# Optimization experiments

Measured on AMD Instinct MI355X. Metric: run time of the kernel, lower is better.

The kernel has to match this reference:

```python
import jax, jax.numpy as jnp
import numpy as np

EPS = 1e-6
N_HEADS = 16
N_KV_HEADS = 4
HEAD_DIM = 128
DIM = 2048
SEQ = 2048
BATCH = 2


def _make_freqs_cis(seqlen, head_dim, theta=10000.0):
    inv = 1.0 / (theta ** (jnp.arange(0, head_dim, 2, dtype=jnp.float32) / head_dim))  # [hd/2]
    t = jnp.arange(seqlen, dtype=jnp.float32)
    ang = jnp.outer(t, inv)  # [seq, hd/2]
    return jnp.stack([jnp.cos(ang), jnp.sin(ang)], axis=-1)  # [seq, hd/2, 2]


def setup_inputs() -> dict:
    key = jax.random.key(0)
    k1, k2, k3 = jax.random.split(key, 3)
    std = 0.02
    x = jax.random.normal(k1, (BATCH, SEQ, DIM), dtype=jnp.float32)
    freqs_cis = _make_freqs_cis(SEQ, HEAD_DIM)
    norm_w = jnp.ones((DIM,), dtype=jnp.float32)
    wqkv_w = jax.random.normal(k2, ((N_HEADS + 2 * N_KV_HEADS) * HEAD_DIM, DIM), dtype=jnp.float32) * std
    wo_w = jax.random.normal(k3, (DIM, N_HEADS * HEAD_DIM), dtype=jnp.float32) * std
    return {"x": x, "freqs_cis": freqs_cis, "norm_w": norm_w, "wqkv_w": wqkv_w, "wo_w": wo_w}


def _rope(t, cos, sin):
    # t: [b, s, h, hd] viewed as pairs; cos/sin: [s, hd/2]
    b, s, h, hd = t.shape
    tr = t.reshape(b, s, h, hd // 2, 2)
    xr, xi = tr[..., 0], tr[..., 1]
    c = cos[None, :, None, :]
    sn = sin[None, :, None, :]
    out_r = xr * c - xi * sn
    out_i = xr * sn + xi * c
    return jnp.stack([out_r, out_i], axis=-1).reshape(b, s, h, hd)


def reference(x, freqs_cis, norm_w, wqkv_w, wo_w):
    bs, seqlen, dim = x.shape
    n_rep = N_HEADS // N_KV_HEADS
    # RMSNorm
    xn = x * jax.lax.rsqrt(jnp.mean(x * x, axis=-1, keepdims=True) + EPS) * norm_w
    # fused QKV projection
    qkv = jnp.einsum('bsd,ed->bse', xn, wqkv_w)
    q_sz = N_HEADS * HEAD_DIM
    kv_sz = N_KV_HEADS * HEAD_DIM
    xq = qkv[..., :q_sz].reshape(bs, seqlen, N_HEADS, HEAD_DIM)
    xk = qkv[..., q_sz:q_sz + kv_sz].reshape(bs, seqlen, N_KV_HEADS, HEAD_DIM)
    xv = qkv[..., q_sz + kv_sz:].reshape(bs, seqlen, N_KV_HEADS, HEAD_DIM)
    cos, sin = freqs_cis[..., 0], freqs_cis[..., 1]
    xq = _rope(xq, cos, sin)
    xk = _rope(xk, cos, sin)
    # GQA: group q heads so kv broadcast replaces repeat_kv materialization
    q = xq.transpose(0, 2, 1, 3).reshape(bs, N_KV_HEADS, n_rep, seqlen, HEAD_DIM)
    k = xk.transpose(0, 2, 1, 3)  # [b, g, s, d]
    v = xv.transpose(0, 2, 1, 3)
    scale = 1.0 / jnp.sqrt(jnp.float32(HEAD_DIM))
    scores = jnp.einsum('bgrqd,bgkd->bgrqk', q, k) * scale
    causal = jnp.tril(jnp.ones((seqlen, seqlen), dtype=bool))
    scores = jnp.where(causal, scores, jnp.finfo(scores.dtype).min)
    probs = jax.nn.softmax(scores, axis=-1)
    out = jnp.einsum('bgrqk,bgkd->bgrqd', probs, v)
    out = out.reshape(bs, N_HEADS, seqlen, HEAD_DIM).transpose(0, 2, 1, 3).reshape(bs, seqlen, N_HEADS * HEAD_DIM)
    return jnp.einsum('bse,de->bsd', out, wo_w)
```

## Files before the change

### kernel.cpp

```cpp
#include <hip/hip_runtime.h>
#include <cstdint>
#include <cstddef>

typedef __bf16 bhalf;
typedef __bf16 bhalf8 __attribute__((ext_vector_type(8)));
typedef __bf16 bhalf4 __attribute__((ext_vector_type(4)));
typedef float f32x4 __attribute__((ext_vector_type(4)));
typedef float f32x16 __attribute__((ext_vector_type(16)));

#define RMS_EPS 1e-6f
#define N_HEADS 16
#define N_KV 4
#define HD 128
#define DIM 2048
#define SEQ 2048
#define BATCH 2

static __device__ __forceinline__ f32x4 mfma16(bhalf8 a, bhalf8 b, f32x4 c) {
    return __builtin_amdgcn_mfma_f32_16x16x32_bf16(a, b, c, 0, 0, 0);
}
static __device__ __forceinline__ f32x16 mfma32(bhalf8 a, bhalf8 b, f32x16 c) {
    return __builtin_amdgcn_mfma_f32_32x32x16_bf16(a, b, c, 0, 0, 0);
}

static __device__ __forceinline__ void gload16(const bhalf* g, bhalf* l) {
    __builtin_amdgcn_global_load_lds((const __attribute__((address_space(1))) unsigned int*)g,
                                     (__attribute__((address_space(3))) unsigned int*)l,
                                     16, 0, 0);
}

static __device__ __forceinline__ unsigned cvt_pk_bf16(float a, float b) {
    unsigned r;
    asm volatile("v_cvt_pk_bf16_f32 %0, %1, %2" : "=v"(r) : "v"(a), "v"(b));
    return r;
}
static __device__ __forceinline__ void plane32_swap(unsigned& a, unsigned& b) {
    asm volatile("v_permlane32_swap_b32 %0, %1" : "+v"(a), "+v"(b));
}

__global__ __launch_bounds__(256) void prep_k(const float* __restrict__ x,
                                              const float* __restrict__ w,
                                              bhalf* __restrict__ xn,
                                              const float* __restrict__ wqkv,
                                              const float* __restrict__ wo,
                                              bhalf* __restrict__ wdst) {
    const int blk = blockIdx.x;
    const int tid = threadIdx.x;
    if (blk < BATCH * SEQ) {
        const int row = blk;
        const float4* xr = (const float4*)(x + (size_t)row * DIM);
        float4 v0 = xr[tid * 2], v1 = xr[tid * 2 + 1];
        float ss = v0.x * v0.x + v0.y * v0.y + v0.z * v0.z + v0.w * v0.w
                 + v1.x * v1.x + v1.y * v1.y + v1.z * v1.z + v1.w * v1.w;
        #pragma unroll
        for (int off = 32; off; off >>= 1) ss += __shfl_xor(ss, off, 64);
        __shared__ float red[4];
        if ((tid & 63) == 0) red[tid >> 6] = ss;
        __syncthreads();
        float tot = red[0] + red[1] + red[2] + red[3];
        float scale = rsqrtf(tot * (1.0f / DIM) + RMS_EPS);
        const float4* wr = (const float4*)w;
        float4 w0 = wr[tid * 2], w1 = wr[tid * 2 + 1];
        bhalf8 o;
        o[0] = (bhalf)(v0.x * scale * w0.x); o[1] = (bhalf)(v0.y * scale * w0.y);
        o[2] = (bhalf)(v0.z * scale * w0.z); o[3] = (bhalf)(v0.w * scale * w0.w);
        o[4] = (bhalf)(v1.x * scale * w1.x); o[5] = (bhalf)(v1.y * scale * w1.y);
        o[6] = (bhalf)(v1.z * scale * w1.z); o[7] = (bhalf)(v1.w * scale * w1.w);
        *(bhalf8*)(xn + (size_t)row * DIM + tid * 8) = o;
    } else {
        size_t i = ((size_t)(blk - BATCH * SEQ) * 256 + tid) * 4;
        const size_t NQ = (size_t)3072 * 2048;
        float4 v = (i < NQ) ? ((const float4*)wqkv)[i >> 2]
                            : ((const float4*)wo)[(i - NQ) >> 2];
        bhalf4 o;
        o[0] = (bhalf)v.x; o[1] = (bhalf)v.y; o[2] = (bhalf)v.z; o[3] = (bhalf)v.w;
        *(bhalf4*)(wdst + i) = o;
    }
}

template <typename OutT>
__global__ __launch_bounds__(512) void gemm8p(const bhalf* __restrict__ A,
                                              const bhalf* __restrict__ B,
                                              OutT* __restrict__ C,
                                              int N, int K) {
    extern __shared__ __align__(16) char smem[];
    const int tid = threadIdx.x;
    const int wid = tid >> 6, lane = tid & 63;
    const int quad = lane >> 4, r16 = lane & 15;
    const int wm = wid >> 2, wn = wid & 3;

    const int nx = N >> 8;
    const int cpx = (int)gridDim.x >> 3;
    const int bs = (int)blockIdx.x;
    const int bid = (bs & 7) * cpx + (bs >> 3);
    const int m0 = (bid / nx) << 8, n0 = (bid % nx) << 8;

    const int srow = wid * 8 + (lane >> 3);
    const int scol = ((lane & 7) ^ ((lane >> 3) & 7)) << 3;
    const bhalf* Asrc = A + (size_t)(m0 + srow) * K + scol;
    const bhalf* Bsrc = B + (size_t)(n0 + srow) * K + scol;
    const size_t r64K = (size_t)64 * K;
    const size_t r128K = (size_t)128 * K;

    const int x7 = r16 & 7;
    const int sl0 = (quad ^ (x7 & 3)) << 4;
    const int ksx = (x7 >> 2) << 6;
    const int k0 = ksx, k1 = 64 ^ ksx;
    const int aoff = (wm << 14) + (r16 << 7) + sl0;
    const int boff = ((2 + (wn >> 1)) << 14) + ((((wn & 1) << 6) + r16) << 7) + sl0;

    f32x4 acc[8][4];
    #pragma unroll
    for (int i = 0; i < 8; ++i)
        #pragma unroll
        for (int j = 0; j < 4; ++j) acc[i][j] = (f32x4)0.0f;

    const int NT = K >> 6;
    const int H = K >> 4;
    int h = 8;

    auto STAGE = [&](int hidx) {
        const int T = hidx >> 2, f = hidx & 3;
        const bhalf* s = ((f < 2) ? Asrc : Bsrc) + ((f & 1) ? r128K : 0) + T * 64;
        char* d = smem + ((T & 1) << 16) + (f << 14) + (wid << 10);
        gload16(s, (bhalf*)d);
        gload16(s + r64K, (bhalf*)(d + 8192));
    };

    #pragma unroll
    for (int i = 0; i < 8; ++i) STAGE(i);
    asm volatile("s_waitcnt vmcnt(8)" ::: "memory");
    __builtin_amdgcn_s_barrier();

    bhalf8 af[4][2], bf[4][2];

    for (int t = 0; t < NT; t += 2) {
        #pragma unroll
        for (int hf = 0; hf < 2; ++hf) {
            char* const bp = smem + (hf << 16);
            #pragma unroll
            for (int i = 0; i < 4; ++i) {
                af[i][0] = *(const bhalf8*)(bp + aoff + i * 2048 + k0);
                af[i][1] = *(const bhalf8*)(bp + aoff + i * 2048 + k1);
            }
            #pragma unroll
            for (int j = 0; j < 2; ++j) {
                bf[j][0] = *(const bhalf8*)(bp + boff + j * 2048 + k0);
                bf[j][1] = *(const bhalf8*)(bp + boff + j * 2048 + k1);
            }
            if ((t > 0 || hf == 1) && h < H) STAGE(h++);
            asm volatile("s_waitcnt lgkmcnt(8)" ::: "memory");
            __builtin_amdgcn_s_barrier();
            __builtin_amdgcn_s_setprio(1);
            #pragma unroll
            for (int i = 0; i < 4; ++i)
                #pragma unroll
                for (int j = 0; j < 2; ++j) {
                    acc[i][j] = mfma16(af[i][0], bf[j][0], acc[i][j]);
                    acc[i][j] = mfma16(af[i][1], bf[j][1], acc[i][j]);
                }
            __builtin_amdgcn_s_setprio(0);
            __builtin_amdgcn_s_barrier();

            #pragma unroll
            for (int j = 2; j < 4; ++j) {
                bf[j][0] = *(const bhalf8*)(bp + boff + j * 2048 + k0);
                bf[j][1] = *(const bhalf8*)(bp + boff + j * 2048 + k1);
            }
            if ((t > 0 || hf == 1) && h < H) STAGE(h++);
            __builtin_amdgcn_s_barrier();
            __builtin_amdgcn_s_setprio(1);
            #pragma unroll
            for (int i = 0; i < 4; ++i)
                #pragma unroll
                for (int j = 2; j < 4; ++j) {
                    acc[i][j] = mfma16(af[i][0], bf[j][0], acc[i][j]);
                    acc[i][j] = mfma16(af[i][1], bf[j][1], acc[i][j]);
                }
            __builtin_amdgcn_s_setprio(0);
            __builtin_amdgcn_s_barrier();

            #pragma unroll
            for (int i = 0; i < 4; ++i) {
                af[i][0] = *(const bhalf8*)(bp + aoff + (i + 4) * 2048 + k0);
                af[i][1] = *(const bhalf8*)(bp + aoff + (i + 4) * 2048 + k1);
            }
            if ((t > 0 || hf == 1) && h < H) STAGE(h++);
            __builtin_amdgcn_s_barrier();
            __builtin_amdgcn_s_setprio(1);
            #pragma unroll
            for (int i = 0; i < 4; ++i)
                #pragma unroll
                for (int j = 0; j < 2; ++j) {
                    acc[i + 4][j] = mfma16(af[i][0], bf[j][0], acc[i + 4][j]);
                    acc[i + 4][j] = mfma16(af[i][1], bf[j][1], acc[i + 4][j]);
                }
            __builtin_amdgcn_s_setprio(0);
            __builtin_amdgcn_s_barrier();

            bool st = (h < H);
            if (st) STAGE(h++);
            __builtin_amdgcn_s_barrier();
            __builtin_amdgcn_s_setprio(1);
            #pragma unroll
            for (int i = 0; i < 4; ++i)
                #pragma unroll
                for (int j = 2; j < 4; ++j) {
                    acc[i + 4][j] = mfma16(af[i][0], bf[j][0], acc[i + 4][j]);
                    acc[i + 4][j] = mfma16(af[i][1], bf[j][1], acc[i + 4][j]);
                }
            __builtin_amdgcn_s_setprio(0);
            if (st) asm volatile("s_waitcnt vmcnt(2)" ::: "memory");
            else    asm volatile("s_waitcnt vmcnt(0)" ::: "memory");
            __builtin_amdgcn_s_barrier();
        }
    }

    #pragma unroll
    for (int i = 0; i < 8; ++i) {
        const int rbase = m0 + wm * 128 + i * 16 + quad * 4;
        #pragma unroll
        for (int rr = 0; rr < 4; ++rr) {
            OutT* crow = C + (size_t)(rbase + rr) * N + n0 + wn * 64 + r16;
            #pragma unroll
            for (int j = 0; j < 4; ++j) crow[j * 16] = (OutT)acc[i][j][rr];
        }
    }
}

template <typename OutT>
__global__ __launch_bounds__(256) void gemm128(const bhalf* __restrict__ A,
                                               const bhalf* __restrict__ B,
                                               OutT* __restrict__ C,
                                               int N, int K) {
    const int tid = threadIdx.x;
    const int w = tid >> 6, lane = tid & 63;
    const int quad = lane >> 4, r16 = lane & 15;
    const int wm = w >> 1, wn = w & 1;

    const int nx = N >> 7;
    const int cpx = (int)gridDim.x >> 3;
    const int bs = (int)blockIdx.x;
    const int bid = (bs & 7) * cpx + (bs >> 3);
    const int m0 = (bid / nx) << 7, n0 = (bid % nx) << 7;

    __shared__ __align__(16) char smem[49152];
    char* const sA = smem;
    char* const sB = smem + 24576;

    const int srow = lane >> 2;
    const int scol = ((lane & 3) ^ (srow & 3)) << 3;
    const bhalf* Ast = A + (size_t)(m0 + w * 16 + srow) * K + scol;
    const bhalf* Bst = B + (size_t)(n0 + w * 16 + srow) * K + scol;
    const size_t r64K = (size_t)64 * K;

    const int xorr = (r16 & 3) << 4;
    const int rdA = (wm * 64 + r16) * 64 + ((quad * 16) ^ xorr);
    const int rdB = (wn * 64 + r16) * 64 + ((quad * 16) ^ xorr);

    f32x4 acc[4][4];
    #pragma unroll
    for (int i = 0; i < 4; ++i)
        #pragma unroll
        for (int j = 0; j < 4; ++j) acc[i][j] = (f32x4)0.0f;

    const int NT = K >> 5;

    #define STG128(t, buf) do {                                                        \
        gload16(Ast + (size_t)(t) * 32,        (bhalf*)(sA + (buf) * 8192 + w * 1024));        \
        gload16(Ast + (size_t)(t) * 32 + r64K, (bhalf*)(sA + (buf) * 8192 + 4096 + w * 1024)); \
        gload16(Bst + (size_t)(t) * 32,        (bhalf*)(sB + (buf) * 8192 + w * 1024));        \
        gload16(Bst + (size_t)(t) * 32 + r64K, (bhalf*)(sB + (buf) * 8192 + 4096 + w * 1024)); \
    } while (0)

    STG128(0, 0);
    STG128(1, 1);

    int cur = 0, c2 = 2;
    for (int t = 0; t < NT; ++t) {
        if (t + 1 < NT) asm volatile("s_waitcnt vmcnt(4)" ::: "memory");
        else            asm volatile("s_waitcnt vmcnt(0)" ::: "memory");
        __builtin_amdgcn_s_barrier();

        char* const bufA = sA + cur * 8192;
        char* const bufB = sB + cur * 8192;
        bhalf8 af[4], bf[4];
        #pragma unroll
        for (int i = 0; i < 4; ++i) af[i] = *(const bhalf8*)(bufA + rdA + i * 1024);
        #pragma unroll
        for (int j = 0; j < 4; ++j) bf[j] = *(const bhalf8*)(bufB + rdB + j * 1024);

        if (t + 2 < NT) STG128(t + 2, c2);

        __builtin_amdgcn_s_setprio(1);
        #pragma unroll
        for (int i = 0; i < 4; ++i)
            #pragma unroll
            for (int j = 0; j < 4; ++j)
                acc[i][j] = mfma16(af[i], bf[j], acc[i][j]);
        __builtin_amdgcn_s_setprio(0);

        cur = (cur == 2) ? 0 : cur + 1;
        c2 = (c2 == 2) ? 0 : c2 + 1;
    }
    #undef STG128

    #pragma unroll
    for (int i = 0; i < 4; ++i) {
        const int rbase = m0 + wm * 64 + i * 16 + quad * 4;
        #pragma unroll
        for (int rr = 0; rr < 4; ++rr) {
            OutT* crow = C + (size_t)(rbase + rr) * N + n0 + wn * 64 + r16;
            #pragma unroll
            for (int j = 0; j < 4; ++j) crow[j * 16] = (OutT)acc[i][j][rr];
        }
    }
}

__global__ __launch_bounds__(256) void rope_k(const bhalf* __restrict__ qkv,
                                              const float* __restrict__ freqs,
                                              bhalf* __restrict__ qb,
                                              bhalf* __restrict__ kb,
                                              bhalf* __restrict__ vt) {
    const int blk = blockIdx.x;
    const int tid = threadIdx.x;
    if (blk < BATCH * SEQ) {
        const int b = blk >> 11, s = blk & 2047;
        const bhalf* row = qkv + (size_t)blk * 3072;
        {
            const int h = tid >> 4, d20 = (tid & 15) * 4;
            bhalf8 e = *(const bhalf8*)(row + h * HD + d20 * 2);
            const float* fp = freqs + (size_t)s * 128 + d20 * 2;
            float4 f0 = *(const float4*)fp;
            float4 f1 = *(const float4*)(fp + 4);
            bhalf8 o;
            o[0] = (bhalf)((float)e[0] * f0.x - (float)e[1] * f0.y);
            o[1] = (bhalf)((float)e[0] * f0.y + (float)e[1] * f0.x);
            o[2] = (bhalf)((float)e[2] * f0.z - (float)e[3] * f0.w);
            o[3] = (bhalf)((float)e[2] * f0.w + (float)e[3] * f0.z);
            o[4] = (bhalf)((float)e[4] * f1.x - (float)e[5] * f1.y);
            o[5] = (bhalf)((float)e[4] * f1.y + (float)e[5] * f1.x);
            o[6] = (bhalf)((float)e[6] * f1.z - (float)e[7] * f1.w);
            o[7] = (bhalf)((float)e[6] * f1.w + (float)e[7] * f1.z);
            *(bhalf8*)(qb + ((size_t)(b * N_HEADS + h) * SEQ + s) * HD + d20 * 2) = o;
        }
        if (tid < 64) {
            const int kh = tid >> 4, d20 = (tid & 15) * 4;
            bhalf8 e = *(const bhalf8*)(row + 2048 + kh * HD + d20 * 2);
            const float* fp = freqs + (size_t)s * 128 + d20 * 2;
            float4 f0 = *(const float4*)fp;
            float4 f1 = *(const float4*)(fp + 4);
            bhalf8 o;
            o[0] = (bhalf)((float)e[0] * f0.x - (float)e[1] * f0.y);
            o[1] = (bhalf)((float)e[0] * f0.y + (float)e[1] * f0.x);
            o[2] = (bhalf)((float)e[2] * f0.z - (float)e[3] * f0.w);
            o[3] = (bhalf)((float)e[2] * f0.w + (float)e[3] * f0.z);
            o[4] = (bhalf)((float)e[4] * f1.x - (float)e[5] * f1.y);
            o[5] = (bhalf)((float)e[4] * f1.y + (float)e[5] * f1.x);
            o[6] = (bhalf)((float)e[6] * f1.z - (float)e[7] * f1.w);
            o[7] = (bhalf)((float)e[6] * f1.w + (float)e[7] * f1.z);
            *(bhalf8*)(kb + ((size_t)(b * N_KV + kh) * SEQ + s) * HD + d20 * 2) = o;
        }
    } else {
        const int vb = blk - BATCH * SEQ;
        const int sc = vb & 31;
        const int kvh = (vb >> 5) & 3;
        const int b = vb >> 7;
        const int s0 = sc * 64;
        __shared__ __align__(16) char lds[64 * 256];

        const int rr = tid >> 4;
        const int slot = tid & 15;
        #pragma unroll
        for (int p = 0; p < 4; ++p) {
            const int s = p * 16 + rr;
            bhalf8 v = *(const bhalf8*)(qkv + (size_t)(b * SEQ + s0 + s) * 3072
                                        + 2560 + kvh * HD + slot * 8);
            *(bhalf8*)(lds + s * 256 + ((slot ^ ((s >> 3) & 7)) << 4)) = v;
        }
        __syncthreads();
        const int j = tid & 7;
        const int d0 = tid >> 3;
        #pragma unroll
        for (int p = 0; p < 4; ++p) {
            const int d = p * 32 + d0;
            bhalf8 o;
            #pragma unroll
            for (int e = 0; e < 8; ++e) {
                const int s = j * 8 + e;
                o[e] = *(const bhalf*)(lds + s * 256 + (((d >> 3) ^ j) << 4) + (d & 7) * 2);
            }
            *(bhalf8*)(vt + ((size_t)(b * N_KV + kvh) * HD + d) * SEQ + s0 + j * 8) = o;
        }
    }
}

__global__ __launch_bounds__(256, 2) void attn_k(const bhalf* __restrict__ qb,
                                                 const bhalf* __restrict__ kb,
                                                 const bhalf* __restrict__ vt,
                                                 bhalf* __restrict__ ob) {
    const int tid = threadIdx.x;
    const int wave = tid >> 6, lane = tid & 63;
    const int l31 = lane & 31, h2 = lane >> 5;
    const int qw = wave & 1, kw = wave >> 1;
    const int bid = ((blockIdx.x & 7) << 6) | ((int)blockIdx.x >> 3);
    const int pair = bid & 15;
    const int hh = (bid >> 4) & 15;
    const int b = bid >> 8;
    const int kvh = hh >> 2;

    __shared__ __align__(16) char smem[33792];
    char* const sK = smem;
    char* const sV = smem + 16384;
    float* const mrg = (float*)smem;

    const bhalf* Kbase = kb + (size_t)(b * N_KV + kvh) * SEQ * HD;
    const bhalf* Vbase = vt + (size_t)(b * N_KV + kvh) * HD * SEQ;
    const float SCL2 = 0.08838834764831845f * 1.4426950408889634f;

    const int mbase = (qw * 64 + lane) * 66;
    const int kr = tid >> 4, kce = (tid & 15) * 8;
    const int vr = tid >> 3, vce = (tid & 7) * 8;
    const int kcB = kce * 2, vcB = vce * 2;
    const int Xl = (h2 << 4) ^ ((l31 & 7) << 4);

    for (int phase = 0; phase < 2; ++phase) {
        const int qt = phase ? (31 - pair) : pair;
        const int qrow = qt * 64 + qw * 32 + l31;
        const int qhi = qt * 64 + qw * 32 + 31;

        const bhalf* qbase = qb + (((size_t)(b * N_HEADS + hh) * SEQ) + qrow) * HD;
        bhalf8 qf[8];
        #pragma unroll
        for (int kk = 0; kk < 8; ++kk) {
            bhalf8 q0 = *(const bhalf8*)(qbase + kk * 16 + h2 * 8);
            #pragma unroll
            for (int e = 0; e < 8; ++e) q0[e] = (bhalf)((float)q0[e] * SCL2);
            qf[kk] = q0;
        }

        f32x16 accO[4];
        #pragma unroll
        for (int dt = 0; dt < 4; ++dt) accO[dt] = (f32x16)0.0f;
        float m_i = -1e30f, l_i = 0.0f;

        bhalf8 kreg[4], vreg[4];
        #pragma unroll
        for (int i = 0; i < 4; ++i) {
            kreg[i] = *(const bhalf8*)(Kbase + (size_t)(kr + 16 * i) * HD + kce);
            vreg[i] = *(const bhalf8*)(Vbase + (size_t)(vr + 32 * i) * SEQ + vce);
        }

        for (int kt = 0; kt <= qt; ++kt) {
            __syncthreads();
            #pragma unroll
            for (int i = 0; i < 4; ++i) {
                const int rk = kr + 16 * i;
                *(bhalf8*)(sK + rk * 256 + (kcB ^ ((rk & 7) << 4))) = kreg[i];
                const int rv = vr + 32 * i;
                *(bhalf8*)(sV + rv * 128 + (vcB ^ ((rv & 7) << 4))) = vreg[i];
            }
            __syncthreads();
            if (kt < qt) {
                const int kn = (kt + 1) * 64;
                #pragma unroll
                for (int i = 0; i < 4; ++i) {
                    kreg[i] = *(const bhalf8*)(Kbase + (size_t)(kn + kr + 16 * i) * HD + kce);
                    vreg[i] = *(const bhalf8*)(Vbase + (size_t)(vr + 32 * i) * SEQ + kn + vce);
                }
            }
            if (qhi < kt * 64 + kw * 32) continue;

            f32x16 accS = (f32x16)0.0f;
            const char* kRow = sK + (kw * 32 + l31) * 256;
            __builtin_amdgcn_s_setprio(1);
            #pragma unroll
            for (int kk = 0; kk < 8; ++kk)
                accS = mfma32(*(const bhalf8*)(kRow + ((kk * 32) ^ Xl)), qf[kk], accS);
            __builtin_amdgcn_s_setprio(0);

            if (kt == qt) {
                #pragma unroll
                for (int r = 0; r < 16; ++r) {
                    const int key = kt * 64 + kw * 32 + (r & 3) + 8 * (r >> 2) + 4 * h2;
                    if (key > qrow) accS[r] = -1e30f;
                }
            }

            float mx = -1e30f;
            #pragma unroll
            for (int r = 0; r < 16; ++r) mx = fmaxf(mx, accS[r]);
            mx = fmaxf(mx, __shfl_xor(mx, 32, 64));

            if (!__all(mx <= m_i + 8.0f)) {
                const float mnew = fmaxf(m_i, mx);
                const float alpha = __builtin_amdgcn_exp2f(m_i - mnew);
                m_i = mnew;
                l_i *= alpha;
                #pragma unroll
                for (int dt = 0; dt < 4; ++dt)
                    #pragma unroll
                    for (int r = 0; r < 16; ++r) accO[dt][r] *= alpha;
            }

            float p[16];
            float rs = 0.0f;
            #pragma unroll
            for (int r = 0; r < 16; ++r) {
                p[r] = __builtin_amdgcn_exp2f(accS[r] - m_i);
                rs += p[r];
            }
            rs += __shfl_xor(rs, 32, 64);
            l_i += rs;

            unsigned X0 = cvt_pk_bf16(p[0],  p[1]);
            unsigned X1 = cvt_pk_bf16(p[2],  p[3]);
            unsigned X2 = cvt_pk_bf16(p[4],  p[5]);
            unsigned X3 = cvt_pk_bf16(p[6],  p[7]);
            unsigned X4 = cvt_pk_bf16(p[8],  p[9]);
            unsigned X5 = cvt_pk_bf16(p[10], p[11]);
            unsigned X6 = cvt_pk_bf16(p[12], p[13]);
            unsigned X7 = cvt_pk_bf16(p[14], p[15]);
            plane32_swap(X0, X2);
            plane32_swap(X1, X3);
            plane32_swap(X4, X6);
            plane32_swap(X5, X7);
            union { unsigned u[8]; bhalf8 h[2]; } pk;
            pk.u[0] = X0; pk.u[1] = X1; pk.u[2] = X2; pk.u[3] = X3;
            pk.u[4] = X4; pk.u[5] = X5; pk.u[6] = X6; pk.u[7] = X7;

            __builtin_amdgcn_s_setprio(1);
            #pragma unroll
            for (int kk2 = 0; kk2 < 2; ++kk2) {
                const int cb = (kw << 6) | (kk2 << 5);
                #pragma unroll
                for (int dt = 0; dt < 4; ++dt) {
                    const bhalf8 vfv = *(const bhalf8*)(sV + (dt * 32 + l31) * 128 + (cb ^ Xl));
                    accO[dt] = mfma32(vfv, pk.h[kk2], accO[dt]);
                }
            }
            __builtin_amdgcn_s_setprio(0);
        }

        __syncthreads();
        if (kw == 1) {
            #pragma unroll
            for (int dt = 0; dt < 4; ++dt)
                #pragma unroll
                for (int r = 0; r < 16; ++r) mrg[mbase + dt * 16 + r] = accO[dt][r];
            mrg[mbase + 64] = m_i;
            mrg[mbase + 65] = l_i;
        }
        __syncthreads();
        if (kw == 0) {
            const float m1 = mrg[mbase + 64];
            const float l1 = mrg[mbase + 65];
            const float m = fmaxf(m_i, m1);
            const float b0 = __builtin_amdgcn_exp2f(m_i - m);
            const float b1 = __builtin_amdgcn_exp2f(m1 - m);
            const float inv = 1.0f / (l_i * b0 + l1 * b1);
            bhalf* obase = ob + ((size_t)b * SEQ + qrow) * (size_t)(N_HEADS * HD) + hh * HD;
            #pragma unroll
            for (int dt = 0; dt < 4; ++dt)
                #pragma unroll
                for (int c = 0; c < 4; ++c) {
                    bhalf4 o4;
                    #pragma unroll
                    for (int rr = 0; rr < 4; ++rr) {
                        const float v = accO[dt][c * 4 + rr] * b0 +
                                        mrg[mbase + dt * 16 + c * 4 + rr] * b1;
                        o4[rr] = (bhalf)(v * inv);
                    }
                    *(bhalf4*)(obase + dt * 32 + c * 8 + h2 * 4) = o4;
                }
        }
    }
}

extern "C" void kernel_launch(void* const* d_in, const int* in_sizes, int n_in,
                              void* d_out, int out_size, void* d_ws, size_t ws_size,
                              hipStream_t stream) {
    const float* x      = (const float*)d_in[0];
    const float* freqs  = (const float*)d_in[1];
    const float* norm_w = (const float*)d_in[2];
    const float* wqkv   = (const float*)d_in[3];
    const float* wo     = (const float*)d_in[4];
    float* out = (float*)d_out;

    char* ws = (char*)d_ws;
    bhalf* wqkv_b = (bhalf*)(ws);
    bhalf* wo_b   = (bhalf*)(ws + 12582912);
    bhalf* xn     = (bhalf*)(ws + 20971520);
    bhalf* qkv    = (bhalf*)(ws + 37748736);
    bhalf* qb     = (bhalf*)(ws + 88080384);
    bhalf* kb     = (bhalf*)(ws + 104857600);
    bhalf* vtb    = (bhalf*)(ws + 109051904);
    bhalf* attn   = (bhalf*)(ws + 113246208);

    static bool attr_done = false;
    if (!attr_done) {
        hipFuncSetAttribute((const void*)gemm8p<bhalf>,
                            hipFuncAttributeMaxDynamicSharedMemorySize, 131072);
        attr_done = true;
    }

    prep_k<<<BATCH * SEQ + 10240, 256, 0, stream>>>(x, norm_w, xn, wqkv, wo, wqkv_b);
    gemm8p<bhalf><<<192, 512, 131072, stream>>>(xn, wqkv_b, qkv, 3072, 2048);
    rope_k<<<BATCH * SEQ + 256, 256, 0, stream>>>(qkv, freqs, qb, kb, vtb);
    attn_k<<<512, 256, 0, stream>>>(qb, kb, vtb, attn);
    gemm128<float><<<512, 256, 0, stream>>>(attn, wo_b, out, 2048, 2048);
}
```

Before: 284.8 us.

## Retile QKV GEMM to 256x192 blocks filling 256 CUs

Replaces the 256x256-tile QKV projection GEMM with a 256x192-tile variant, so the 4096x3072 output maps to 256 blocks instead of 192 and matches the CU count better. The software pipeline is reworked to single-k-tile double buffering with 7 staged loads per tile and new LDS offsets. Each warp now covers 48 columns, which means fewer MFMAs per LDS read and some loss of per-block data reuse.

```diff
diff --git a/kernel.cpp b/kernel.cpp
--- a/kernel.cpp
+++ b/kernel.cpp
@@ -78,142 +78,141 @@
     }
 }
 
-template <typename OutT>
-__global__ __launch_bounds__(512) void gemm8p(const bhalf* __restrict__ A,
-                                              const bhalf* __restrict__ B,
-                                              OutT* __restrict__ C,
-                                              int N, int K) {
+__global__ __launch_bounds__(512) void gemmq(const bhalf* __restrict__ A,
+                                             const bhalf* __restrict__ B,
+                                             bhalf* __restrict__ C,
+                                             int N, int K) {
     extern __shared__ __align__(16) char smem[];
     const int tid = threadIdx.x;
     const int wid = tid >> 6, lane = tid & 63;
     const int quad = lane >> 4, r16 = lane & 15;
     const int wm = wid >> 2, wn = wid & 3;
 
-    const int nx = N >> 8;
+    const int nx = N / 192;
     const int cpx = (int)gridDim.x >> 3;
     const int bs = (int)blockIdx.x;
     const int bid = (bs & 7) * cpx + (bs >> 3);
-    const int m0 = (bid / nx) << 8, n0 = (bid % nx) << 8;
+    const int m0 = (bid / nx) << 8, n0 = (bid % nx) * 192;
 
     const int srow = wid * 8 + (lane >> 3);
     const int scol = ((lane & 7) ^ ((lane >> 3) & 7)) << 3;
     const bhalf* Asrc = A + (size_t)(m0 + srow) * K + scol;
     const bhalf* Bsrc = B + (size_t)(n0 + srow) * K + scol;
-    const size_t r64K = (size_t)64 * K;
-    const size_t r128K = (size_t)128 * K;
 
     const int x7 = r16 & 7;
     const int sl0 = (quad ^ (x7 & 3)) << 4;
     const int ksx = (x7 >> 2) << 6;
     const int k0 = ksx, k1 = 64 ^ ksx;
-    const int aoff = (wm << 14) + (r16 << 7) + sl0;
-    const int boff = ((2 + (wn >> 1)) << 14) + ((((wn & 1) << 6) + r16) << 7) + sl0;
-
-    f32x4 acc[8][4];
+    int aofs[8], bofs[3];
+    #pragma unroll
+    for (int i = 0; i < 8; ++i) {
+        const int g = wm * 128 + i * 16 + r16;
+        aofs[i] = ((g >> 6) << 13) + ((g & 63) << 7) + sl0;
+    }
+    #pragma unroll
+    for (int j = 0; j < 3; ++j) {
+        const int g = wn * 48 + j * 16 + r16;
+        bofs[j] = 32768 + ((g >> 6) << 13) + ((g & 63) << 7) + sl0;
+    }
+
+    auto STG = [&](int T, const bhalf* base, int rowb, int lreg) {
+        gload16(base + (size_t)rowb * K + (size_t)T * 64,
+                (bhalf*)(smem + (T & 1) * 57344 + lreg + wid * 1024));
+    };
+
+    f32x4 acc[8][3];
     #pragma unroll
     for (int i = 0; i < 8; ++i)
         #pragma unroll
-        for (int j = 0; j < 4; ++j) acc[i][j] = (f32x4)0.0f;
+        for (int j = 0; j < 3; ++j) acc[i][j] = (f32x4)0.0f;
 
     const int NT = K >> 6;
-    const int H = K >> 4;
-    int h = 8;
-
-    auto STAGE = [&](int hidx) {
-        const int T = hidx >> 2, f = hidx & 3;
-        const bhalf* s = ((f < 2) ? Asrc : Bsrc) + ((f & 1) ? r128K : 0) + T * 64;
-        char* d = smem + ((T & 1) << 16) + (f << 14) + (wid << 10);
-        gload16(s, (bhalf*)d);
-        gload16(s + r64K, (bhalf*)(d + 8192));
-    };
 
     #pragma unroll
-    for (int i = 0; i < 8; ++i) STAGE(i);
-    asm volatile("s_waitcnt vmcnt(8)" ::: "memory");
+    for (int T = 0; T < 2; ++T) {
+        STG(T, Bsrc, 0, 32768); STG(T, Bsrc, 64, 40960); STG(T, Bsrc, 128, 49152);
+        STG(T, Asrc, 0, 0);     STG(T, Asrc, 128, 16384);
+        STG(T, Asrc, 64, 8192); STG(T, Asrc, 192, 24576);
+    }
+    asm volatile("s_waitcnt vmcnt(7)" ::: "memory");
     __builtin_amdgcn_s_barrier();
 
-    bhalf8 af[4][2], bf[4][2];
-
-    for (int t = 0; t < NT; t += 2) {
-        #pragma unroll
-        for (int hf = 0; hf < 2; ++hf) {
-            char* const bp = smem + (hf << 16);
-            #pragma unroll
-            for (int i = 0; i < 4; ++i) {
-                af[i][0] = *(const bhalf8*)(bp + aoff + i * 2048 + k0);
-                af[i][1] = *(const bhalf8*)(bp + aoff + i * 2048 + k1);
-            }
+    for (int t = 0; t < NT; ++t) {
+        char* const bp = smem + (t & 1) * 57344;
+        const bool stg = (t > 0) && (t + 1 < NT);
+        const int tn = t + 1;
+        const bool last = (t + 1 == NT);
+
+        bhalf8 af[4][2], bf[3][2];
+        #pragma unroll
+        for (int i = 0; i < 4; ++i) {
+            af[i][0] = *(const bhalf8*)(bp + aofs[i] + k0);
+            af[i][1] = *(const bhalf8*)(bp + aofs[i] + k1);
+        }
+        #pragma unroll
+        for (int j = 0; j < 2; ++j) {
+            bf[j][0] = *(const bhalf8*)(bp + bofs[j] + k0);
+            bf[j][1] = *(const bhalf8*)(bp + bofs[j] + k1);
+        }
+        if (stg) { STG(tn, Bsrc, 0, 32768); STG(tn, Bsrc, 64, 40960); }
+        asm volatile("s_waitcnt lgkmcnt(8)" ::: "memory");
+        __builtin_amdgcn_s_barrier();
+        __builtin_amdgcn_s_setprio(1);
+        #pragma unroll
+        for (int i = 0; i < 4; ++i)
             #pragma unroll
             for (int j = 0; j < 2; ++j) {
-                bf[j][0] = *(const bhalf8*)(bp + boff + j * 2048 + k0);
-                bf[j][1] = *(const bhalf8*)(bp + boff + j * 2048 + k1);
-            }
-            if ((t > 0 || hf == 1) && h < H) STAGE(h++);
-            asm volatile("s_waitcnt lgkmcnt(8)" ::: "memory");
-            __builtin_amdgcn_s_barrier();
-            __builtin_amdgcn_s_setprio(1);
-            #pragma unroll
-            for (int i = 0; i < 4; ++i)
-                #pragma unroll
-                for (int j = 0; j < 2; ++j) {
-                    acc[i][j] = mfma16(af[i][0], bf[j][0], acc[i][j]);
-                    acc[i][j] = mfma16(af[i][1], bf[j][1], acc[i][j]);
-                }
-            __builtin_amdgcn_s_setprio(0);
-            __builtin_amdgcn_s_barrier();
-
-            #pragma unroll
-            for (int j = 2; j < 4; ++j) {
-                bf[j][0] = *(const bhalf8*)(bp + boff + j * 2048 + k0);
-                bf[j][1] = *(const bhalf8*)(bp + boff + j * 2048 + k1);
-            }
-            if ((t > 0 || hf == 1) && h < H) STAGE(h++);
-            __builtin_amdgcn_s_barrier();
-            __builtin_amdgcn_s_setprio(1);
-            #pragma unroll
-            for (int i = 0; i < 4; ++i)
-                #pragma unroll
-                for (int j = 2; j < 4; ++j) {
-                    acc[i][j] = mfma16(af[i][0], bf[j][0], acc[i][j]);
-                    acc[i][j] = mfma16(af[i][1], bf[j][1], acc[i][j]);
-                }
-            __builtin_amdgcn_s_setprio(0);
-            __builtin_amdgcn_s_barrier();
-
-            #pragma unroll
-            for (int i = 0; i < 4; ++i) {
-                af[i][0] = *(const bhalf8*)(bp + aoff + (i + 4) * 2048 + k0);
-                af[i][1] = *(const bhalf8*)(bp + aoff + (i + 4) * 2048 + k1);
-            }
-            if ((t > 0 || hf == 1) && h < H) STAGE(h++);
-            __builtin_amdgcn_s_barrier();
-            __builtin_amdgcn_s_setprio(1);
-            #pragma unroll
-            for (int i = 0; i < 4; ++i)
-                #pragma unroll
-                for (int j = 0; j < 2; ++j) {
-                    acc[i + 4][j] = mfma16(af[i][0], bf[j][0], acc[i + 4][j]);
-                    acc[i + 4][j] = mfma16(af[i][1], bf[j][1], acc[i + 4][j]);
-                }
-            __builtin_amdgcn_s_setprio(0);
-            __builtin_amdgcn_s_barrier();
-
-            bool st = (h < H);
-            if (st) STAGE(h++);
-            __builtin_amdgcn_s_barrier();
-            __builtin_amdgcn_s_setprio(1);
-            #pragma unroll
-            for (int i = 0; i < 4; ++i)
-                #pragma unroll
-                for (int j = 2; j < 4; ++j) {
-                    acc[i + 4][j] = mfma16(af[i][0], bf[j][0], acc[i + 4][j]);
-                    acc[i + 4][j] = mfma16(af[i][1], bf[j][1], acc[i + 4][j]);
-                }
-            __builtin_amdgcn_s_setprio(0);
-            if (st) asm volatile("s_waitcnt vmcnt(2)" ::: "memory");
-            else    asm volatile("s_waitcnt vmcnt(0)" ::: "memory");
-            __builtin_amdgcn_s_barrier();
-        }
+                acc[i][j] = mfma16(af[i][0], bf[j][0], acc[i][j]);
+                acc[i][j] = mfma16(af[i][1], bf[j][1], acc[i][j]);
+            }
+        __builtin_amdgcn_s_setprio(0);
+        __builtin_amdgcn_s_barrier();
+
+        bf[2][0] = *(const bhalf8*)(bp + bofs[2] + k0);
+        bf[2][1] = *(const bhalf8*)(bp + bofs[2] + k1);
+        if (stg) { STG(tn, Bsrc, 128, 49152); STG(tn, Asrc, 0, 0); }
+        __builtin_amdgcn_s_barrier();
+        __builtin_amdgcn_s_setprio(1);
+        #pragma unroll
+        for (int i = 0; i < 4; ++i) {
+            acc[i][2] = mfma16(af[i][0], bf[2][0], acc[i][2]);
+            acc[i][2] = mfma16(af[i][1], bf[2][1], acc[i][2]);
+        }
+        __builtin_amdgcn_s_setprio(0);
+        if (!last) asm volatile("s_waitcnt vmcnt(4)" ::: "memory");
+        else       asm volatile("s_waitcnt vmcnt(0)" ::: "memory");
+        __builtin_amdgcn_s_barrier();
+
+        #pragma unroll
+        for (int i = 0; i < 4; ++i) {
+            af[i][0] = *(const bhalf8*)(bp + aofs[i + 4] + k0);
+            af[i][1] = *(const bhalf8*)(bp + aofs[i + 4] + k1);
+        }
+        if (stg) { STG(tn, Asrc, 128, 16384); STG(tn, Asrc, 64, 8192); }
+        __builtin_amdgcn_s_barrier();
+        __builtin_amdgcn_s_setprio(1);
+        #pragma unroll
+        for (int i = 0; i < 4; ++i)
+            #pragma unroll
+            for (int j = 0; j < 2; ++j) {
+                acc[i + 4][j] = mfma16(af[i][0], bf[j][0], acc[i + 4][j]);
+                acc[i + 4][j] = mfma16(af[i][1], bf[j][1], acc[i + 4][j]);
+            }
+        __builtin_amdgcn_s_setprio(0);
+        __builtin_amdgcn_s_barrier();
+
+        if (stg) STG(tn, Asrc, 192, 24576);
+        __builtin_amdgcn_s_barrier();
+        __builtin_amdgcn_s_setprio(1);
+        #pragma unroll
+        for (int i = 0; i < 4; ++i) {
+            acc[i + 4][2] = mfma16(af[i][0], bf[2][0], acc[i + 4][2]);
+            acc[i + 4][2] = mfma16(af[i][1], bf[2][1], acc[i + 4][2]);
+        }
+        __builtin_amdgcn_s_setprio(0);
+        if (!last) asm volatile("s_waitcnt vmcnt(1)" ::: "memory");
+        else       asm volatile("s_waitcnt vmcnt(0)" ::: "memory");
+        __builtin_amdgcn_s_barrier();
     }
 
     #pragma unroll
@@ -221,9 +220,9 @@
         const int rbase = m0 + wm * 128 + i * 16 + quad * 4;
         #pragma unroll
         for (int rr = 0; rr < 4; ++rr) {
-            OutT* crow = C + (size_t)(rbase + rr) * N + n0 + wn * 64 + r16;
-            #pragma unroll
-            for (int j = 0; j < 4; ++j) crow[j * 16] = (OutT)acc[i][j][rr];
+            bhalf* crow = C + (size_t)(rbase + rr) * N + n0 + wn * 48 + r16;
+            #pragma unroll
+            for (int j = 0; j < 3; ++j) crow[j * 16] = (bhalf)acc[i][j][rr];
         }
     }
 }
@@ -599,13 +598,13 @@
 
     static bool attr_done = false;
     if (!attr_done) {
-        hipFuncSetAttribute((const void*)gemm8p<bhalf>,
-                            hipFuncAttributeMaxDynamicSharedMemorySize, 131072);
+        hipFuncSetAttribute((const void*)gemmq,
+                            hipFuncAttributeMaxDynamicSharedMemorySize, 114688);
         attr_done = true;
     }
 
     prep_k<<<BATCH * SEQ + 10240, 256, 0, stream>>>(x, norm_w, xn, wqkv, wo, wqkv_b);
-    gemm8p<bhalf><<<192, 512, 131072, stream>>>(xn, wqkv_b, qkv, 3072, 2048);
+    gemmq<<<256, 512, 114688, stream>>>(xn, wqkv_b, qkv, 3072, 2048);
     rope_k<<<BATCH * SEQ + 256, 256, 0, stream>>>(qkv, freqs, qb, kb, vtb);
     attn_k<<<512, 256, 0, stream>>>(qb, kb, vtb, attn);
     gemm128<float><<<512, 256, 0, stream>>>(attn, wo_b, out, 2048, 2048);
```

Result: no change. 280.8 us (-1.4%).
